# Kernel tuning notes

Hardware: AMD Instinct MI355X
Metric: run time of the kernel (lower is better)

## Reference

```python
import jax, jax.numpy as jnp
import numpy as np

NUM_EMBEDDINGS = 1024
EMBEDDING_DIM = 64
COMMITMENT_COST = 0.25


def setup_inputs() -> dict:
    key = jax.random.key(0)
    k1, k2 = jax.random.split(key)
    z_e = jax.random.normal(k1, (32, 64, 64, 64), dtype=jnp.float32)  # NHWC
    lim = 1.0 / NUM_EMBEDDINGS
    embeddings = jax.random.uniform(
        k2, (NUM_EMBEDDINGS, EMBEDDING_DIM), minval=-lim, maxval=lim, dtype=jnp.float32
    )
    return {"z_e": z_e, "embeddings": embeddings}


def reference(z_e, embeddings):
    D = embeddings.shape[1]
    # Faithful to the TF module: NHWC -> NCHW, then flatten into rows of length D.
    z = jnp.transpose(z_e, (0, 3, 1, 2))            # [B, C, H, W]
    flat = z.reshape(-1, D)                          # [N, D]
    # Squared distances via GEMM (argmin of ||.||^2 == argmin of ||.||); avoids the [N, K, D] tensor.
    d2 = (
        jnp.sum(flat * flat, axis=-1, keepdims=True)
        - 2.0 * flat @ embeddings.T
        + jnp.sum(embeddings * embeddings, axis=-1)
    )                                                # [N, K]
    indices = jnp.argmin(d2, axis=1)                 # [N]
    z_q = embeddings[indices].reshape(z.shape)       # [B, C, H, W]
    z_q_st = z_q + jax.lax.stop_gradient(z - z_q)    # straight-through estimator
    e_latent_loss = jnp.mean((jax.lax.stop_gradient(z_q) - z) ** 2)
    q_latent_loss = jnp.mean((z_q_st - jax.lax.stop_gradient(z)) ** 2)
    loss = q_latent_loss + COMMITMENT_COST * e_latent_loss
    return jnp.transpose(z_q_st, (0, 2, 3, 1)), indices, loss
```

## Files before the change

### kernel.cpp

```cpp
#include <hip/hip_runtime.h>


#define N_Z 8388608
#define N_IDX 131072
#define K_EMB 1024
#define D_EMB 64
#define EPS_GAP 1.25e-4f

typedef __attribute__((ext_vector_type(8))) short bf16x8;
typedef __attribute__((ext_vector_type(4))) float f32x4;

__device__ __forceinline__ unsigned short f2bf(float f) {
  unsigned u = __builtin_bit_cast(unsigned, f);
  unsigned r = 0x7fffu + ((u >> 16) & 1u);
  return (unsigned short)((u + r) >> 16);
}
__device__ __forceinline__ float bf2f(unsigned short b) {
  return __builtin_bit_cast(float, (unsigned)b << 16);
}

__global__ __launch_bounds__(256) void ek2f_kernel(
    const float* __restrict__ emb, float* __restrict__ ek2f) {
  int k = blockIdx.x * 256 + threadIdx.x;
  const float* row = emb + (size_t)k * D_EMB;
  float s = 0.0f;
  for (int d = 0; d < D_EMB; d++) {
    float e = row[d];
    float sq = e * e;
    asm volatile("" : "+v"(sq));
    s = s + sq;
  }
  ek2f[k] = s;
}

__global__ __launch_bounds__(256) void ebf_prep_kernel(
    const float* __restrict__ emb, unsigned short* __restrict__ ehi,
    unsigned short* __restrict__ elo) {
  int gid = blockIdx.x * 256 + threadIdx.x;
  int k = gid >> 3, oct = gid & 7;
  const float* src = emb + (size_t)k * 64 + oct * 8;
  int kt = k >> 4, sp = oct >> 2, l = (oct & 3) * 16 + (k & 15);
  size_t off = ((size_t)((kt * 2 + sp) * 64 + l)) * 8;
  bf16x8 h8, l8;
  #pragma unroll
  for (int i = 0; i < 8; i++) {
    float v = src[i];
    unsigned short hb = f2bf(v);
    float lf = v - bf2f(hb);
    h8[i] = (short)hb;
    l8[i] = (short)f2bf(lf);
  }
  *(bf16x8*)(ehi + off) = h8;
  *(bf16x8*)(elo + off) = l8;
}

__global__ __launch_bounds__(256) void vq_main_kernel(
    const float* __restrict__ z, const float* __restrict__ emb,
    const float* __restrict__ ek2g,
    const unsigned short* __restrict__ ehi_g,
    const unsigned short* __restrict__ elo_g,
    float* __restrict__ out_idx, double* __restrict__ loss_acc) {
  __shared__ __align__(16) float zts[64][64];
  __shared__ __align__(16) unsigned short lhi[2][4096];
  __shared__ __align__(16) unsigned short llo[2][4096];
  __shared__ float sk2[K_EMB];
  __shared__ float sa[64];
  __shared__ int sidx[64];
  __shared__ int sflag[64];
  __shared__ double lred[16];
  __shared__ float wrv[4];
  __shared__ int wri[4];

  const int t = threadIdx.x;
  const int bid = blockIdx.x;
  const int l = t & 63;
  const int wv = t >> 6;
  const int cb = wv * 16;

  const float4* zt4 = (const float4*)(z + (size_t)bid * 4096);
  #pragma unroll
  for (int q = 0; q < 4; q++) {
    int p = t + q * 256;
    float4 v = zt4[p];
    *(float4*)&zts[p >> 4][(p & 15) * 4] = v;
  }
  #pragma unroll
  for (int q = 0; q < 4; q++) sk2[t + q * 256] = ek2g[t + q * 256];
  {
    const int tt = t & 127;
    const uint4* src = (t < 128) ? (const uint4*)ehi_g : (const uint4*)elo_g;
    unsigned short* dst = (t < 128) ? lhi[0] : llo[0];
    #pragma unroll
    for (int q = 0; q < 4; q++)
      *(uint4*)&dst[tt * 32 + q * 8] = src[tt * 4 + q];
  }
  __syncthreads();

  if (t < 64) {
    float a = 0.0f;
    for (int w = 0; w < 64; w++) {
      float zf = zts[w][t];
      float sq = zf * zf;
      asm volatile("" : "+v"(sq));
      a = a + sq;
    }
    sa[t] = a;
  }

  bf16x8 zh0, zh1, zl0, zl1;
  {
    const int crow = cb + (l & 15);
    const int wb = (l >> 4) * 8;
    #pragma unroll
    for (int i = 0; i < 8; i++) {
      float zf = zts[wb + i][crow];
      unsigned short hb = f2bf(zf);
      float lf = zf - bf2f(hb);
      zh0[i] = (short)hb; zl0[i] = (short)f2bf(lf);
      float zf1 = zts[32 + wb + i][crow];
      unsigned short hb1 = f2bf(zf1);
      float lf1 = zf1 - bf2f(hb1);
      zh1[i] = (short)hb1; zl1[i] = (short)f2bf(lf1);
    }
  }
  __syncthreads();

  float A_[4];
  #pragma unroll
  for (int i = 0; i < 4; i++) A_[i] = sa[cb + ((l >> 4) & 3) * 4 + i];

  float m1[4], m2[4];
  int i1[4];
  #pragma unroll
  for (int i = 0; i < 4; i++) { m1[i] = 3.0e38f; m2[i] = 3.0e38f; i1[i] = 0; }

  for (int ch = 0; ch < 16; ch++) {
    const int cur = ch & 1;
    uint4 pf[4];
    if (ch < 15) {
      const int tt = t & 127;
      const uint4* src = (t < 128) ? (const uint4*)ehi_g : (const uint4*)elo_g;
      #pragma unroll
      for (int q = 0; q < 4; q++)
        pf[q] = src[(size_t)(ch + 1) * 512 + tt * 4 + q];
    }

    #pragma unroll
    for (int t4 = 0; t4 < 4; t4++) {
      const int fb = (t4 * 2) * 64 * 8 + l * 8;
      bf16x8 bh0 = *(const bf16x8*)&lhi[cur][fb];
      bf16x8 bh1 = *(const bf16x8*)&lhi[cur][fb + 512];
      bf16x8 bl0 = *(const bf16x8*)&llo[cur][fb];
      bf16x8 bl1 = *(const bf16x8*)&llo[cur][fb + 512];
      f32x4 acc = {0.f, 0.f, 0.f, 0.f};
      acc = __builtin_amdgcn_mfma_f32_16x16x32_bf16(zh0, bh0, acc, 0, 0, 0);
      acc = __builtin_amdgcn_mfma_f32_16x16x32_bf16(zh1, bh1, acc, 0, 0, 0);
      acc = __builtin_amdgcn_mfma_f32_16x16x32_bf16(zh0, bl0, acc, 0, 0, 0);
      acc = __builtin_amdgcn_mfma_f32_16x16x32_bf16(zh1, bl1, acc, 0, 0, 0);
      acc = __builtin_amdgcn_mfma_f32_16x16x32_bf16(zl0, bh0, acc, 0, 0, 0);
      acc = __builtin_amdgcn_mfma_f32_16x16x32_bf16(zl1, bh1, acc, 0, 0, 0);

      const int k = ch * 64 + t4 * 16 + (l & 15);
      const float ck = sk2[k];
      #pragma unroll
      for (int i = 0; i < 4; i++) {
        float sc = fmaf(-2.0f, acc[i], A_[i]) + ck;
        if (sc < m1[i]) { m2[i] = m1[i]; m1[i] = sc; i1[i] = k; }
        else            { m2[i] = fminf(m2[i], sc); }
      }
    }

    if (ch < 15) {
      const int tt = t & 127;
      unsigned short* dst = (t < 128) ? lhi[cur ^ 1] : llo[cur ^ 1];
      #pragma unroll
      for (int q = 0; q < 4; q++)
        *(uint4*)&dst[tt * 32 + q * 8] = pf[q];
    }
    __syncthreads();
  }

  #pragma unroll
  for (int ci = 0; ci < 4; ci++) {
    float v1 = m1[ci], v2 = m2[ci];
    int ix = i1[ci];
    #pragma unroll
    for (int m = 8; m; m >>= 1) {
      float ov1 = __shfl_xor(v1, m, 16);
      int oi1 = __shfl_xor(ix, m, 16);
      float ov2 = __shfl_xor(v2, m, 16);
      if (ov1 < v1)      { v2 = fminf(v1, ov2); v1 = ov1; ix = oi1; }
      else if (ov1 > v1) { v2 = fminf(v2, ov1); }
      else               { v2 = v1; ix = min(ix, oi1); }
    }
    m1[ci] = v1; m2[ci] = v2; i1[ci] = ix;
  }
  if ((t & 15) == 0) {
    #pragma unroll
    for (int ci = 0; ci < 4; ci++) {
      int c = (t >> 4) * 4 + ci;
      sidx[c] = i1[ci];
      sflag[c] = (m2[ci] - m1[ci] <= EPS_GAP) ? 1 : 0;
    }
  }
  __syncthreads();

  for (int c = 0; c < 64; c++) {
    if (!sflag[c]) continue;
    float A = sa[c];
    float lm = 3.0e38f;
    int li = 0;
    #pragma unroll
    for (int r = 0; r < 4; r++) {
      int k = t + 256 * r;
      double B = 0.0;
      const float4* e4 = (const float4*)(emb + (size_t)k * 64);
      for (int w4 = 0; w4 < 16; w4++) {
        float4 e = e4[w4];
        B += (double)zts[w4 * 4 + 0][c] * (double)e.x;
        B += (double)zts[w4 * 4 + 1][c] * (double)e.y;
        B += (double)zts[w4 * 4 + 2][c] * (double)e.z;
        B += (double)zts[w4 * 4 + 3][c] * (double)e.w;
      }
      float Bf = (float)B;
      float t1 = A - 2.0f * Bf;
      float sc = t1 + sk2[k];
      if (sc < lm) { lm = sc; li = k; }
    }
    #pragma unroll
    for (int m = 32; m; m >>= 1) {
      float ov = __shfl_xor(lm, m);
      int oi = __shfl_xor(li, m);
      if (ov < lm || (ov == lm && oi < li)) { lm = ov; li = oi; }
    }
    if ((t & 63) == 0) { wrv[t >> 6] = lm; wri[t >> 6] = li; }
    __syncthreads();
    if (t == 0) {
      float bv = wrv[0]; int bi = wri[0];
      #pragma unroll
      for (int q = 1; q < 4; q++) {
        if (wrv[q] < bv || (wrv[q] == bv && wri[q] < bi)) { bv = wrv[q]; bi = wri[q]; }
      }
      sidx[c] = bi;
    }
    __syncthreads();
  }
  __syncthreads();

  const int b = bid >> 6, h = bid & 63;
  if (t < 64) out_idx[(size_t)b * 4096 + t * 64 + h] = (float)sidx[t];

  double ls = 0.0;
  #pragma unroll
  for (int ci = 0; ci < 4; ci++) {
    int c = (t >> 4) * 4 + ci;
    const float* er = emb + (size_t)sidx[c] * 64;
    #pragma unroll
    for (int s = 0; s < 4; s++) {
      int w = (t & 15) + 16 * s;
      double d = (double)zts[w][c] - (double)er[w];
      ls += d * d;
    }
  }
  #pragma unroll
  for (int m = 8; m; m >>= 1) ls += __shfl_xor(ls, m, 16);
  if ((t & 15) == 0) lred[t >> 4] = ls;
  __syncthreads();
  if (t == 0) {
    double s = 0.0;
    #pragma unroll
    for (int q = 0; q < 16; q++) s += lred[q];
    atomicAdd(loss_acc, s);
  }
}

__global__ void loss_final_kernel(const double* __restrict__ acc,
                                  float* __restrict__ out_loss) {
  *out_loss = (float)(0.25 * (*acc) / (double)N_Z);
}

extern "C" void kernel_launch(void* const* d_in, const int* in_sizes, int n_in,
                              void* d_out, int out_size, void* d_ws, size_t ws_size,
                              hipStream_t stream) {
  const float* z = (const float*)d_in[0];
  const float* emb = (const float*)d_in[1];
  float* out = (float*)d_out;

  float* ek2f = (float*)d_ws;
  double* lacc = (double*)((char*)d_ws + 4096);
  unsigned short* ehi = (unsigned short*)((char*)d_ws + 8192);
  unsigned short* elo = (unsigned short*)((char*)d_ws + 8192 + 131072);

  (void)hipMemsetAsync(lacc, 0, sizeof(double), stream);
  (void)hipMemcpyAsync(out, z, (size_t)N_Z * sizeof(float),
                       hipMemcpyDeviceToDevice, stream);
  ek2f_kernel<<<4, 256, 0, stream>>>(emb, ek2f);
  ebf_prep_kernel<<<32, 256, 0, stream>>>(emb, ehi, elo);
  vq_main_kernel<<<2048, 256, 0, stream>>>(z, emb, ek2f, ehi, elo,
                                           out + N_Z, lacc);
  loss_final_kernel<<<1, 1, 0, stream>>>(lacc, out + N_Z + N_IDX);
}
```

Before: 447.9 us.

## Process two z tiles per block, read codebook from global, fuse output copy

```diff
diff --git a/kernel.cpp b/kernel.cpp
--- a/kernel.cpp
+++ b/kernel.cpp
@@ -54,212 +54,219 @@
   *(bf16x8*)(elo + off) = l8;
 }
 
+#define MFMA_BF16 __builtin_amdgcn_mfma_f32_16x16x32_bf16
+
 __global__ __launch_bounds__(256) void vq_main_kernel(
     const float* __restrict__ z, const float* __restrict__ emb,
     const float* __restrict__ ek2g,
     const unsigned short* __restrict__ ehi_g,
     const unsigned short* __restrict__ elo_g,
-    float* __restrict__ out_idx, double* __restrict__ loss_acc) {
-  __shared__ __align__(16) float zts[64][64];
-  __shared__ __align__(16) unsigned short lhi[2][4096];
-  __shared__ __align__(16) unsigned short llo[2][4096];
+    float* __restrict__ out0, float* __restrict__ out_idx,
+    double* __restrict__ loss_acc) {
+  __shared__ __align__(16) float zts[2][64][64];
   __shared__ float sk2[K_EMB];
-  __shared__ float sa[64];
-  __shared__ int sidx[64];
-  __shared__ int sflag[64];
+  __shared__ float sa[2][64];
+  __shared__ int sidx[2][64];
+  __shared__ int sflag[2][64];
   __shared__ double lred[16];
   __shared__ float wrv[4];
   __shared__ int wri[4];
 
   const int t = threadIdx.x;
-  const int bid = blockIdx.x;
+  const int bid2 = blockIdx.x;
   const int l = t & 63;
-  const int wv = t >> 6;
-  const int cb = wv * 16;
-
-  const float4* zt4 = (const float4*)(z + (size_t)bid * 4096);
-  #pragma unroll
-  for (int q = 0; q < 4; q++) {
+  const int cb = (t >> 6) * 16;
+
+  const float4* zt4 = (const float4*)(z + (size_t)bid2 * 8192);
+  float4* o4 = (float4*)(out0 + (size_t)bid2 * 8192);
+  #pragma unroll
+  for (int q = 0; q < 8; q++) {
     int p = t + q * 256;
     float4 v = zt4[p];
-    *(float4*)&zts[p >> 4][(p & 15) * 4] = v;
+    int ti = p >> 10, p4 = p & 1023;
+    *(float4*)&zts[ti][p4 >> 4][(p4 & 15) * 4] = v;
+    o4[p] = v;
   }
   #pragma unroll
   for (int q = 0; q < 4; q++) sk2[t + q * 256] = ek2g[t + q * 256];
-  {
-    const int tt = t & 127;
-    const uint4* src = (t < 128) ? (const uint4*)ehi_g : (const uint4*)elo_g;
-    unsigned short* dst = (t < 128) ? lhi[0] : llo[0];
-    #pragma unroll
-    for (int q = 0; q < 4; q++)
-      *(uint4*)&dst[tt * 32 + q * 8] = src[tt * 4 + q];
-  }
-  __syncthreads();
-
-  if (t < 64) {
+  __syncthreads();
+
+  if (t < 128) {
+    int ti = t >> 6, cc = t & 63;
     float a = 0.0f;
     for (int w = 0; w < 64; w++) {
-      float zf = zts[w][t];
+      float zf = zts[ti][w][cc];
       float sq = zf * zf;
       asm volatile("" : "+v"(sq));
       a = a + sq;
     }
-    sa[t] = a;
-  }
-
-  bf16x8 zh0, zh1, zl0, zl1;
+    sa[ti][cc] = a;
+  }
+
+  bf16x8 zh0_0, zh1_0, zl0_0, zl1_0, zh0_1, zh1_1, zl0_1, zl1_1;
   {
     const int crow = cb + (l & 15);
     const int wb = (l >> 4) * 8;
     #pragma unroll
     for (int i = 0; i < 8; i++) {
-      float zf = zts[wb + i][crow];
-      unsigned short hb = f2bf(zf);
-      float lf = zf - bf2f(hb);
-      zh0[i] = (short)hb; zl0[i] = (short)f2bf(lf);
-      float zf1 = zts[32 + wb + i][crow];
-      unsigned short hb1 = f2bf(zf1);
-      float lf1 = zf1 - bf2f(hb1);
-      zh1[i] = (short)hb1; zl1[i] = (short)f2bf(lf1);
-    }
-  }
-  __syncthreads();
-
-  float A_[4];
-  #pragma unroll
-  for (int i = 0; i < 4; i++) A_[i] = sa[cb + ((l >> 4) & 3) * 4 + i];
-
-  float m1[4], m2[4];
-  int i1[4];
-  #pragma unroll
-  for (int i = 0; i < 4; i++) { m1[i] = 3.0e38f; m2[i] = 3.0e38f; i1[i] = 0; }
+      float a0 = zts[0][wb + i][crow];
+      unsigned short h0 = f2bf(a0);
+      zh0_0[i] = (short)h0; zl0_0[i] = (short)f2bf(a0 - bf2f(h0));
+      float a1 = zts[0][32 + wb + i][crow];
+      unsigned short h1 = f2bf(a1);
+      zh1_0[i] = (short)h1; zl1_0[i] = (short)f2bf(a1 - bf2f(h1));
+      float b0 = zts[1][wb + i][crow];
+      unsigned short g0 = f2bf(b0);
+      zh0_1[i] = (short)g0; zl0_1[i] = (short)f2bf(b0 - bf2f(g0));
+      float b1 = zts[1][32 + wb + i][crow];
+      unsigned short g1 = f2bf(b1);
+      zh1_1[i] = (short)g1; zl1_1[i] = (short)f2bf(b1 - bf2f(g1));
+    }
+  }
+  __syncthreads();
+
+  float A0_[4], A1_[4];
+  #pragma unroll
+  for (int i = 0; i < 4; i++) {
+    A0_[i] = sa[0][cb + (l >> 4) * 4 + i];
+    A1_[i] = sa[1][cb + (l >> 4) * 4 + i];
+  }
+
+  float m1[2][4], m2[2][4];
+  int i1[2][4];
+  #pragma unroll
+  for (int ti = 0; ti < 2; ti++)
+    #pragma unroll
+    for (int i = 0; i < 4; i++) { m1[ti][i] = 3.0e38f; m2[ti][i] = 3.0e38f; i1[ti][i] = 0; }
 
   for (int ch = 0; ch < 16; ch++) {
-    const int cur = ch & 1;
-    uint4 pf[4];
-    if (ch < 15) {
-      const int tt = t & 127;
-      const uint4* src = (t < 128) ? (const uint4*)ehi_g : (const uint4*)elo_g;
-      #pragma unroll
-      for (int q = 0; q < 4; q++)
-        pf[q] = src[(size_t)(ch + 1) * 512 + tt * 4 + q];
-    }
-
     #pragma unroll
     for (int t4 = 0; t4 < 4; t4++) {
-      const int fb = (t4 * 2) * 64 * 8 + l * 8;
-      bf16x8 bh0 = *(const bf16x8*)&lhi[cur][fb];
-      bf16x8 bh1 = *(const bf16x8*)&lhi[cur][fb + 512];
-      bf16x8 bl0 = *(const bf16x8*)&llo[cur][fb];
-      bf16x8 bl1 = *(const bf16x8*)&llo[cur][fb + 512];
-      f32x4 acc = {0.f, 0.f, 0.f, 0.f};
-      acc = __builtin_amdgcn_mfma_f32_16x16x32_bf16(zh0, bh0, acc, 0, 0, 0);
-      acc = __builtin_amdgcn_mfma_f32_16x16x32_bf16(zh1, bh1, acc, 0, 0, 0);
-      acc = __builtin_amdgcn_mfma_f32_16x16x32_bf16(zh0, bl0, acc, 0, 0, 0);
-      acc = __builtin_amdgcn_mfma_f32_16x16x32_bf16(zh1, bl1, acc, 0, 0, 0);
-      acc = __builtin_amdgcn_mfma_f32_16x16x32_bf16(zl0, bh0, acc, 0, 0, 0);
-      acc = __builtin_amdgcn_mfma_f32_16x16x32_bf16(zl1, bh1, acc, 0, 0, 0);
-
-      const int k = ch * 64 + t4 * 16 + (l & 15);
+      const int kt = ch * 4 + t4;
+      const size_t fo = (size_t)kt * 1024 + (size_t)l * 8;
+      bf16x8 bh0 = *(const bf16x8*)(ehi_g + fo);
+      bf16x8 bh1 = *(const bf16x8*)(ehi_g + fo + 512);
+      bf16x8 bl0 = *(const bf16x8*)(elo_g + fo);
+      bf16x8 bl1 = *(const bf16x8*)(elo_g + fo + 512);
+
+      f32x4 a0 = {0.f, 0.f, 0.f, 0.f}, a1 = {0.f, 0.f, 0.f, 0.f};
+      a0 = MFMA_BF16(zh0_0, bh0, a0, 0, 0, 0);
+      a1 = MFMA_BF16(zh0_1, bh0, a1, 0, 0, 0);
+      a0 = MFMA_BF16(zh1_0, bh1, a0, 0, 0, 0);
+      a1 = MFMA_BF16(zh1_1, bh1, a1, 0, 0, 0);
+      a0 = MFMA_BF16(zh0_0, bl0, a0, 0, 0, 0);
+      a1 = MFMA_BF16(zh0_1, bl0, a1, 0, 0, 0);
+      a0 = MFMA_BF16(zh1_0, bl1, a0, 0, 0, 0);
+      a1 = MFMA_BF16(zh1_1, bl1, a1, 0, 0, 0);
+      a0 = MFMA_BF16(zl0_0, bh0, a0, 0, 0, 0);
+      a1 = MFMA_BF16(zl0_1, bh0, a1, 0, 0, 0);
+      a0 = MFMA_BF16(zl1_0, bh1, a0, 0, 0, 0);
+      a1 = MFMA_BF16(zl1_1, bh1, a1, 0, 0, 0);
+
+      const int k = kt * 16 + (l & 15);
       const float ck = sk2[k];
       #pragma unroll
       for (int i = 0; i < 4; i++) {
-        float sc = fmaf(-2.0f, acc[i], A_[i]) + ck;
-        if (sc < m1[i]) { m2[i] = m1[i]; m1[i] = sc; i1[i] = k; }
-        else            { m2[i] = fminf(m2[i], sc); }
-      }
-    }
-
-    if (ch < 15) {
-      const int tt = t & 127;
-      unsigned short* dst = (t < 128) ? lhi[cur ^ 1] : llo[cur ^ 1];
-      #pragma unroll
-      for (int q = 0; q < 4; q++)
-        *(uint4*)&dst[tt * 32 + q * 8] = pf[q];
-    }
-    __syncthreads();
-  }
-
-  #pragma unroll
-  for (int ci = 0; ci < 4; ci++) {
-    float v1 = m1[ci], v2 = m2[ci];
-    int ix = i1[ci];
-    #pragma unroll
-    for (int m = 8; m; m >>= 1) {
-      float ov1 = __shfl_xor(v1, m, 16);
-      int oi1 = __shfl_xor(ix, m, 16);
-      float ov2 = __shfl_xor(v2, m, 16);
-      if (ov1 < v1)      { v2 = fminf(v1, ov2); v1 = ov1; ix = oi1; }
-      else if (ov1 > v1) { v2 = fminf(v2, ov1); }
-      else               { v2 = v1; ix = min(ix, oi1); }
-    }
-    m1[ci] = v1; m2[ci] = v2; i1[ci] = ix;
-  }
-  if ((t & 15) == 0) {
+        float sc0 = fmaf(-2.0f, a0[i], A0_[i]) + ck;
+        if (sc0 < m1[0][i]) { m2[0][i] = m1[0][i]; m1[0][i] = sc0; i1[0][i] = k; }
+        else                { m2[0][i] = fminf(m2[0][i], sc0); }
+        float sc1 = fmaf(-2.0f, a1[i], A1_[i]) + ck;
+        if (sc1 < m1[1][i]) { m2[1][i] = m1[1][i]; m1[1][i] = sc1; i1[1][i] = k; }
+        else                { m2[1][i] = fminf(m2[1][i], sc1); }
+      }
+    }
+  }
+
+  #pragma unroll
+  for (int ti = 0; ti < 2; ti++) {
+    #pragma unroll
+    for (int ci = 0; ci < 4; ci++) {
+      float v1 = m1[ti][ci], v2 = m2[ti][ci];
+      int ix = i1[ti][ci];
+      #pragma unroll
+      for (int m = 8; m; m >>= 1) {
+        float ov1 = __shfl_xor(v1, m, 16);
+        int oi1 = __shfl_xor(ix, m, 16);
+        float ov2 = __shfl_xor(v2, m, 16);
+        if (ov1 < v1)      { v2 = fminf(v1, ov2); v1 = ov1; ix = oi1; }
+        else if (ov1 > v1) { v2 = fminf(v2, ov1); }
+        else               { v2 = v1; ix = min(ix, oi1); }
+      }
+      if ((l & 15) == 0) {
+        int c = cb + (l >> 4) * 4 + ci;
+        sidx[ti][c] = ix;
+        sflag[ti][c] = (v2 - v1 <= EPS_GAP) ? 1 : 0;
+      }
+    }
+  }
+  __syncthreads();
+
+  #pragma unroll 1
+  for (int ti = 0; ti < 2; ti++) {
+    #pragma unroll 1
+    for (int c = 0; c < 64; c++) {
+      if (!sflag[ti][c]) continue;
+      float A = sa[ti][c];
+      float lm = 3.0e38f;
+      int li = 0;
+      #pragma unroll
+      for (int r = 0; r < 4; r++) {
+        int k = t + 256 * r;
+        double B = 0.0;
+        const float4* e4 = (const float4*)(emb + (size_t)k * 64);
+        for (int w4 = 0; w4 < 16; w4++) {
+          float4 e = e4[w4];
+          B += (double)zts[ti][w4 * 4 + 0][c] * (double)e.x;
+          B += (double)zts[ti][w4 * 4 + 1][c] * (double)e.y;
+          B += (double)zts[ti][w4 * 4 + 2][c] * (double)e.z;
+          B += (double)zts[ti][w4 * 4 + 3][c] * (double)e.w;
+        }
+        float Bf = (float)B;
+        float t1 = A - 2.0f * Bf;
+        float sc = t1 + sk2[k];
+        if (sc < lm) { lm = sc; li = k; }
+      }
+      #pragma unroll
+      for (int m = 32; m; m >>= 1) {
+        float ov = __shfl_xor(lm, m);
+        int oi = __shfl_xor(li, m);
+        if (ov < lm || (ov == lm && oi < li)) { lm = ov; li = oi; }
+      }
+      if ((t & 63) == 0) { wrv[t >> 6] = lm; wri[t >> 6] = li; }
+      __syncthreads();
+      if (t == 0) {
+        float bv = wrv[0]; int bi = wri[0];
+        #pragma unroll
+        for (int q = 1; q < 4; q++) {
+          if (wrv[q] < bv || (wrv[q] == bv && wri[q] < bi)) { bv = wrv[q]; bi = wri[q]; }
+        }
+        sidx[ti][c] = bi;
+      }
+      __syncthreads();
+    }
+  }
+  __syncthreads();
+
+  if (t < 128) {
+    int ti = t >> 6, cc = t & 63;
+    int tile = bid2 * 2 + ti;
+    int b = tile >> 6, h = tile & 63;
+    out_idx[(size_t)b * 4096 + cc * 64 + h] = (float)sidx[ti][cc];
+  }
+
+  double ls = 0.0;
+  #pragma unroll
+  for (int ti = 0; ti < 2; ti++) {
     #pragma unroll
     for (int ci = 0; ci < 4; ci++) {
       int c = (t >> 4) * 4 + ci;
-      sidx[c] = i1[ci];
-      sflag[c] = (m2[ci] - m1[ci] <= EPS_GAP) ? 1 : 0;
-    }
-  }
-  __syncthreads();
-
-  for (int c = 0; c < 64; c++) {
-    if (!sflag[c]) continue;
-    float A = sa[c];
-    float lm = 3.0e38f;
-    int li = 0;
-    #pragma unroll
-    for (int r = 0; r < 4; r++) {
-      int k = t + 256 * r;
-      double B = 0.0;
-      const float4* e4 = (const float4*)(emb + (size_t)k * 64);
-      for (int w4 = 0; w4 < 16; w4++) {
-        float4 e = e4[w4];
-        B += (double)zts[w4 * 4 + 0][c] * (double)e.x;
-        B += (double)zts[w4 * 4 + 1][c] * (double)e.y;
-        B += (double)zts[w4 * 4 + 2][c] * (double)e.z;
-        B += (double)zts[w4 * 4 + 3][c] * (double)e.w;
-      }
-      float Bf = (float)B;
-      float t1 = A - 2.0f * Bf;
-      float sc = t1 + sk2[k];
-      if (sc < lm) { lm = sc; li = k; }
-    }
-    #pragma unroll
-    for (int m = 32; m; m >>= 1) {
-      float ov = __shfl_xor(lm, m);
-      int oi = __shfl_xor(li, m);
-      if (ov < lm || (ov == lm && oi < li)) { lm = ov; li = oi; }
-    }
-    if ((t & 63) == 0) { wrv[t >> 6] = lm; wri[t >> 6] = li; }
-    __syncthreads();
-    if (t == 0) {
-      float bv = wrv[0]; int bi = wri[0];
-      #pragma unroll
-      for (int q = 1; q < 4; q++) {
-        if (wrv[q] < bv || (wrv[q] == bv && wri[q] < bi)) { bv = wrv[q]; bi = wri[q]; }
-      }
-      sidx[c] = bi;
-    }
-    __syncthreads();
-  }
-  __syncthreads();
-
-  const int b = bid >> 6, h = bid & 63;
-  if (t < 64) out_idx[(size_t)b * 4096 + t * 64 + h] = (float)sidx[t];
-
-  double ls = 0.0;
-  #pragma unroll
-  for (int ci = 0; ci < 4; ci++) {
-    int c = (t >> 4) * 4 + ci;
-    const float* er = emb + (size_t)sidx[c] * 64;
-    #pragma unroll
-    for (int s = 0; s < 4; s++) {
-      int w = (t & 15) + 16 * s;
-      double d = (double)zts[w][c] - (double)er[w];
-      ls += d * d;
+      const float* er = emb + (size_t)sidx[ti][c] * 64;
+      #pragma unroll
+      for (int s = 0; s < 4; s++) {
+        int w = (t & 15) + 16 * s;
+        double d = (double)zts[ti][w][c] - (double)er[w];
+        ls += d * d;
+      }
     }
   }
   #pragma unroll
@@ -292,11 +299,9 @@
   unsigned short* elo = (unsigned short*)((char*)d_ws + 8192 + 131072);
 
   (void)hipMemsetAsync(lacc, 0, sizeof(double), stream);
-  (void)hipMemcpyAsync(out, z, (size_t)N_Z * sizeof(float),
-                       hipMemcpyDeviceToDevice, stream);
   ek2f_kernel<<<4, 256, 0, stream>>>(emb, ek2f);
   ebf_prep_kernel<<<32, 256, 0, stream>>>(emb, ehi, elo);
-  vq_main_kernel<<<2048, 256, 0, stream>>>(z, emb, ek2f, ehi, elo,
-                                           out + N_Z, lacc);
+  vq_main_kernel<<<1024, 256, 0, stream>>>(z, emb, ek2f, ehi, elo,
+                                           out, out + N_Z, lacc);
   loss_final_kernel<<<1, 1, 0, stream>>>(lacc, out + N_Z + N_IDX);
 }
```

Measured after the change: 439.7 us. Within noise of the previous version (-1.8%).
